# Kernel optimization log

Hardware: AMD Instinct MI355X
Metric: run time of the kernel (lower is better)

Reference implementation:

```python
import jax, jax.numpy as jnp
import numpy as np

B, T, C, NH = 2, 2048, 1024, 16
HD = C // NH  # 64


def _ln(x, g, b, eps=1e-5):
    m = x.mean(-1, keepdims=True)
    v = ((x - m) ** 2).mean(-1, keepdims=True)
    return (x - m) / jnp.sqrt(v + eps) * g + b


def _ff(x, w1, b1, w2, b2):
    # Linear -> exact (erf) GELU -> Linear; dropout=0 (identity)
    return jax.nn.gelu(x @ w1 + b1, approximate=False) @ w2 + b2


def setup_inputs() -> dict:
    key = jax.random.key(0)
    ks = jax.random.split(key, 16)
    s = 0.02
    f32 = jnp.float32
    return {
        "x": jax.random.normal(ks[0], (B, T, C), f32),
        # SelfAttn qkv projection (torch Linear stored transposed: (in, out))
        "w_attn": jax.random.normal(ks[1], (C, 3 * C), f32) * s,
        "b_attn": jnp.zeros((3 * C,), f32),
        # SelfAttn's internal FeedForward
        "wa1": jax.random.normal(ks[2], (C, 4 * C), f32) * s,
        "ba1": jnp.zeros((4 * C,), f32),
        "wa2": jax.random.normal(ks[3], (4 * C, C), f32) * s,
        "ba2": jnp.zeros((C,), f32),
        # Block ln1
        "g1": jnp.ones((C,), f32),
        "be1": jnp.zeros((C,), f32),
        # Block FeedForward
        "wf1": jax.random.normal(ks[4], (C, 4 * C), f32) * s,
        "bf1": jnp.zeros((4 * C,), f32),
        "wf2": jax.random.normal(ks[5], (4 * C, C), f32) * s,
        "bf2": jnp.zeros((C,), f32),
        # Block ln2
        "g2": jnp.ones((C,), f32),
        "be2": jnp.zeros((C,), f32),
    }


def reference(x, w_attn, b_attn, wa1, ba1, wa2, ba2, g1, be1,
              wf1, bf1, wf2, bf2, g2, be2):
    Bx, Tx, Cx = x.shape
    qkv = x @ w_attn + b_attn  # (B, T, 3C)
    # NOTE: original splits as K, Q, V (in that order)
    K, Q, V = jnp.split(qkv, 3, axis=-1)

    def heads(t):  # (B, T, C) -> (B, NH, T, HD)
        return t.reshape(Bx, Tx, NH, HD).transpose(0, 2, 1, 3)

    Q, K, V = heads(Q), heads(K), heads(V)
    att = jnp.einsum('bhqd,bhkd->bhqk', Q, K) / np.float32(np.sqrt(HD))
    mask = jnp.tril(jnp.ones((Tx, Tx), bool))  # causal
    att = jnp.where(mask, att, -jnp.inf)
    att = jax.nn.softmax(att, axis=-1)
    y = jnp.einsum('bhqk,bhkd->bhqd', att, V)
    y = y.transpose(0, 2, 1, 3).reshape(Bx, Tx, Cx)
    # SelfAttn applies its own FeedForward (no output projection)
    y = _ff(y, wa1, ba1, wa2, ba2)
    # Block: post-sublayer LayerNorm, additive residuals
    x = x + _ln(y, g1, be1)
    x = x + _ln(_ff(x, wf1, bf1, wf2, bf2), g2, be2)
    return x
```

## Files before the change

### kernel.cpp

```cpp
#include <hip/hip_runtime.h>
#include <hip/hip_bf16.h>
#include <math.h>

#define Bz 2
#define Tz 2048
#define Cz 1024
#define NHz 16
#define HDz 64
#define Mz (Bz*Tz)

typedef unsigned short u16;
typedef __attribute__((ext_vector_type(8))) short bf16x8;
typedef __attribute__((ext_vector_type(4))) float f32x4;

__device__ __forceinline__ float bf2f(u16 u){
  union { unsigned int i; float f; } v; v.i = ((unsigned int)u) << 16; return v.f;
}
__device__ __forceinline__ u16 f2bf(float f){
  union { float f; unsigned int i; } v; v.f = f;
  return (u16)((v.i + 0x7fffu + ((v.i >> 16) & 1u)) >> 16);
}
__device__ __forceinline__ unsigned pack_bf_trunc(float a, float b){
  union { float f; unsigned u; } ua, ub; ua.f = a; ub.f = b;
  return (ua.u >> 16) | (ub.u & 0xffff0000u);
}
__device__ __forceinline__ float gelu_fast(float x){
  float x3 = x * x * x;
  float z2 = 1.5957691216057308f * (x + 0.044715f * x3);
  float e  = __expf(z2);
  float t  = 1.f - 2.f / (e + 1.f);
  return 0.5f * x * (1.f + t);
}

__device__ __forceinline__ void glds16(const void* g, void* l){
  __builtin_amdgcn_global_load_lds(
      (const __attribute__((address_space(1))) void*)g,
      (__attribute__((address_space(3))) void*)l, 16, 0, 0);
}

__device__ __forceinline__ void pbar(){
  asm volatile("" ::: "memory");
  __builtin_amdgcn_s_barrier();
  asm volatile("" ::: "memory");
}
#define VMCNT(n) asm volatile("s_waitcnt vmcnt(" #n ")" ::: "memory")

__global__ __launch_bounds__(256) void cast4_kernel(const float* __restrict__ in,
                                                    u16* __restrict__ out, int n4){
  int i = blockIdx.x * 256 + threadIdx.x;
  if (i < n4) {
    float4 v = ((const float4*)in)[i];
    u16 t[4] = { f2bf(v.x), f2bf(v.y), f2bf(v.z), f2bf(v.w) };
    *(uint2*)&out[(size_t)i * 4] = *(const uint2*)t;
  }
}

__global__ __launch_bounds__(256) void transpose5_kernel(
    const float* __restrict__ s0, const float* __restrict__ s1,
    const float* __restrict__ s2, const float* __restrict__ s3,
    const float* __restrict__ s4,
    u16* __restrict__ d0, u16* __restrict__ d1, u16* __restrict__ d2,
    u16* __restrict__ d3, u16* __restrict__ d4){
  __shared__ float tile[32][33];
  const int t = blockIdx.x;
  const float* src; u16* dst; int K, N, local;
  if (t < 3072)       { src = s0; dst = d0; K = 1024; N = 3072; local = t; }
  else if (t < 7168)  { src = s1; dst = d1; K = 1024; N = 4096; local = t - 3072; }
  else if (t < 11264) { src = s2; dst = d2; K = 4096; N = 1024; local = t - 7168; }
  else if (t < 15360) { src = s3; dst = d3; K = 1024; N = 4096; local = t - 11264; }
  else                { src = s4; dst = d4; K = 4096; N = 1024; local = t - 15360; }
  const int NT = N >> 5;
  const int kb = (local / NT) * 32, nb = (local % NT) * 32;
  const int tx = threadIdx.x & 31, ty = threadIdx.x >> 5;
  #pragma unroll
  for (int r = ty; r < 32; r += 8)
    tile[r][tx] = src[(size_t)(kb + r) * N + nb + tx];
  __syncthreads();
  #pragma unroll
  for (int r = ty; r < 32; r += 8)
    dst[(size_t)(nb + r) * K + kb + tx] = f2bf(tile[tx][r]);
}

template<int ACT, int KLEN>
__global__ __launch_bounds__(512, 2) void gemm256_kernel(const u16* __restrict__ A,
                                                         const u16* __restrict__ Bt,
                                                         const float* __restrict__ bias,
                                                         u16* __restrict__ ob,
                                                         int N, int lda){
  __shared__ __align__(16) u16 As[2][256 * 64];
  __shared__ __align__(16) u16 Bs[2][256 * 64];
  const int tid  = threadIdx.x;
  const int lane = tid & 63;
  const int wave = tid >> 6;
  const int cc = lane & 15, quad = lane >> 4;
  const int wm = (wave >> 2) * 128;
  const int wn = (wave & 3) * 64;

  int flat = blockIdx.x + gridDim.x * blockIdx.y;
  const int nwg = gridDim.x * gridDim.y;
  flat = (flat & 7) * (nwg >> 3) + (flat >> 3);
  const int m0 = (flat & 15) * 256;
  const int n0 = (flat >> 4) * 256;

  const u16* Ak  = A  + (size_t)blockIdx.z * KLEN;
  const u16* Btk = Bt + (size_t)blockIdx.z * KLEN;

  int srow[2], scol[2];
  #pragma unroll
  for (int rnd = 0; rnd < 2; ++rnd) {
    const int ci = tid + rnd * 512;
    const int r = ci >> 3, cg = ci & 7;
    srow[rnd] = r;
    scol[rnd] = (cg ^ (r & 7)) * 8;
  }
  int colsw[2];
  #pragma unroll
  for (int s = 0; s < 2; ++s)
    colsw[s] = (s * 32 + quad * 8) ^ ((cc & 7) << 3);

  const auto stA = [&](int h, int t) {
    u16* dst = &As[t & 1][h * 8192];
    const u16* src = Ak + (size_t)(m0 + h * 128) * lda + t * 64;
    #pragma unroll
    for (int rnd = 0; rnd < 2; ++rnd)
      glds16(src + (size_t)srow[rnd] * lda + scol[rnd], dst + (tid + rnd * 512) * 8);
  };
  const auto stB = [&](int h, int t) {
    u16* dst = &Bs[t & 1][h * 8192];
    const u16* src = Btk + (size_t)(n0 + h * 128) * lda + t * 64;
    #pragma unroll
    for (int rnd = 0; rnd < 2; ++rnd)
      glds16(src + (size_t)srow[rnd] * lda + scol[rnd], dst + (tid + rnd * 512) * 8);
  };

  bf16x8 af[4][2];
  bf16x8 bfr[2][2][2];
  f32x4 acc[2][2][4][2] = {};

  const auto rdA = [&](int qa, int bsel) {
    #pragma unroll
    for (int f = 0; f < 4; ++f)
      #pragma unroll
      for (int s = 0; s < 2; ++s)
        af[f][s] = *(const bf16x8*)&As[bsel][(wm + qa * 64 + f * 16 + cc) * 64 + colsw[s]];
  };
  const auto rdB = [&](int qb, int bsel) {
    #pragma unroll
    for (int f = 0; f < 2; ++f)
      #pragma unroll
      for (int s = 0; s < 2; ++s)
        bfr[qb][f][s] = *(const bf16x8*)&Bs[bsel][(wn + qb * 32 + f * 16 + cc) * 64 + colsw[s]];
  };
  const auto mf16 = [&](int qa, int qb) {
    __builtin_amdgcn_s_setprio(1);
    #pragma unroll
    for (int s = 0; s < 2; ++s)
      #pragma unroll
      for (int am = 0; am < 4; ++am)
        #pragma unroll
        for (int bn = 0; bn < 2; ++bn)
          acc[qa][qb][am][bn] = __builtin_amdgcn_mfma_f32_16x16x32_bf16(
              af[am][s], bfr[qb][bn][s], acc[qa][qb][am][bn], 0, 0, 0);
    __builtin_amdgcn_s_setprio(0);
  };

  stB(0, 0); stB(1, 0); stA(0, 0); stA(1, 0);
  stB(0, 1); stB(1, 1);
  VMCNT(4);
  pbar();

  constexpr int nIter = KLEN >> 7;
  for (int i = 0; i < nIter; ++i) {
    const int t = 2 * i;
    const bool more = (i + 1 < nIter);
    rdA(0, 0); rdB(0, 0); stA(0, t + 1);
    pbar(); mf16(0, 0); pbar();
    rdB(1, 0); stA(1, t + 1);
    pbar(); mf16(0, 1); pbar();
    rdA(1, 0); if (more) stB(0, t + 2);
    pbar(); mf16(1, 1); pbar();
    if (more) stB(1, t + 2);
    pbar(); mf16(1, 0);
    if (more) { VMCNT(4); } else { VMCNT(0); }
    pbar();
    rdA(0, 1); rdB(0, 1); if (more) stA(0, t + 2);
    pbar(); mf16(0, 0); pbar();
    rdB(1, 1); if (more) stA(1, t + 2);
    pbar(); mf16(0, 1); pbar();
    rdA(1, 1); if (more) stB(0, t + 3);
    pbar(); mf16(1, 1); pbar();
    if (more) stB(1, t + 3);
    pbar(); mf16(1, 0);
    if (more) { VMCNT(4); }
    pbar();
  }

  u16* eb = (u16*)As;
  u16* obz = ob + (size_t)blockIdx.z * ((size_t)Mz * N);
  const float* bp = (blockIdx.z == 0) ? bias : nullptr;
  #pragma unroll
  for (int pass = 0; pass < 4; ++pass) {
    pbar();
    if (wm == (pass >> 1) * 128) {
      constexpr int dummy = 0; (void)dummy;
      const int qaa = pass & 1;
      #pragma unroll
      for (int qb = 0; qb < 2; ++qb)
        #pragma unroll
        for (int bn = 0; bn < 2; ++bn) {
          const int col = wn + qb * 32 + bn * 16 + cc;
          const float bv = bp ? bp[n0 + col] : 0.f;
          #pragma unroll
          for (int am = 0; am < 4; ++am)
            #pragma unroll
            for (int r = 0; r < 4; ++r) {
              const int rl = am * 16 + quad * 4 + r;
              float v = acc[qaa][qb][am][bn][r] + bv;
              if (ACT == 1) v = gelu_fast(v);
              eb[rl * 256 + (((col * 2) ^ ((rl & 7) << 4)) >> 1)] = f2bf(v);
            }
        }
    }
    pbar();
    #pragma unroll
    for (int c2 = 0; c2 < 4; ++c2) {
      const int byteoff = (tid + c2 * 512) * 16;
      const int rl = byteoff >> 9;
      const int cb = byteoff & 511;
      bf16x8 vv = *(const bf16x8*)((const char*)eb + rl * 512 + (cb ^ ((rl & 7) << 4)));
      *(bf16x8*)((char*)obz + ((size_t)(m0 + pass * 64 + rl) * N + n0) * 2 + cb) = vv;
    }
  }
}

__global__ __launch_bounds__(256) void vtrans_kernel(const u16* __restrict__ qkv,
                                                     u16* __restrict__ Vtb){
  __shared__ u16 Vl[64 * 72];
  const int tid = threadIdx.x;
  const int t0 = blockIdx.x * 64, h = blockIdx.y, b = blockIdx.z;
  const int bh = b * NHz + h;
  #pragma unroll
  for (int it = 0; it < 2; it++) {
    int c = tid + it * 256;
    int row = c >> 3, g = c & 7;
    *(uint4*)&Vl[row * 72 + g * 8] =
        *(const uint4*)(qkv + (size_t)(b * Tz + t0 + row) * (3 * Cz) + 2 * Cz + h * 64 + g * 8);
  }
  __syncthreads();
  #pragma unroll
  for (int it = 0; it < 2; it++) {
    int c = tid + it * 256;
    int d = c >> 3, tg = c & 7;
    u16 tmp[8];
    #pragma unroll
    for (int e = 0; e < 8; e++) tmp[e] = Vl[(tg * 8 + e) * 72 + d];
    *(uint4*)&Vtb[((size_t)bh * 64 + d) * Tz + t0 + tg * 8] = *(const uint4*)tmp;
  }
}

__global__ __launch_bounds__(256) void attn_kernel(const u16* __restrict__ qkv,
                                                   const u16* __restrict__ Vtb,
                                                   u16* __restrict__ y){
  __shared__ __align__(16) u16 KV[2][2][64 * 64];
  __shared__ __align__(16) u16 Ps[64 * 72];
  const int tid = threadIdx.x;
  const int lane = tid & 63, wave = tid >> 6;
  const int cc = lane & 15, quad = lane >> 4;
  const int flat = blockIdx.x;
  const int xcd = flat & 7, slot = flat >> 3;
  const int bhg = xcd * 4 + (slot >> 4);
  const int qtp = slot & 15;
  const int h = bhg & 15, b = bhg >> 4;
  const int bh = b * NHz + h;
  const size_t rowb = (size_t)b * Tz;
  const int wq0 = wave * 16;

  int foff[4][2];
  const int sw0 = (quad ^ (cc & 7)) * 8;
  const int sw1 = ((4 + quad) ^ (cc & 7)) * 8;
  #pragma unroll
  for (int t = 0; t < 4; ++t) {
    foff[t][0] = (t * 16 + cc) * 64 + sw0;
    foff[t][1] = (t * 16 + cc) * 64 + sw1;
  }
  const int pswb = (wq0 + cc) * 72 + quad * 4;
  const int psr0 = (wq0 + cc) * 72 + quad * 8;
  const int psr1 = (wq0 + cc) * 72 + 32 + quad * 8;

  auto stage = [&](int i, int bsel) {
    const int k0s = i * 64;
    #pragma unroll
    for (int it = 0; it < 2; ++it) {
      int ci = tid + it * 256;
      int row = ci >> 3, g = ci & 7;
      int gs = g ^ (row & 7);
      glds16(qkv + (rowb + k0s + row) * (3 * Cz) + h * 64 + gs * 8, &KV[bsel][0][ci * 8]);
      glds16(Vtb + ((size_t)bh * 64 + row) * Tz + k0s + gs * 8,     &KV[bsel][1][ci * 8]);
    }
  };

  for (int ph = 0; ph < 2; ++ph) {
    const int qt = ph ? (31 - qtp) : qtp;
    const int q0t = qt * 64 + wq0;
    const int nkt = qt + 1;
    const int wqmax = q0t + 15;

    bf16x8 qf[2];
    #pragma unroll
    for (int s = 0; s < 2; ++s)
      qf[s] = *(const bf16x8*)(qkv + (rowb + q0t + cc) * (3 * Cz)
                               + Cz + h * 64 + s * 32 + quad * 8);
    f32x4 acc[4] = {};
    float lp = 0.f;

    if (ph) __syncthreads();
    stage(0, 0);

    for (int i = 0; i < nkt; ++i) {
      __syncthreads();
      if (i + 1 < nkt) stage(i + 1, (i + 1) & 1);
      const int sel = i & 1;
      const u16* Kl = KV[sel][0];
      const u16* Vl = KV[sel][1];
      const int k0 = i * 64;
      if (k0 > wqmax) continue;

      bf16x8 kf[4][2];
      #pragma unroll
      for (int kt = 0; kt < 4; ++kt) {
        kf[kt][0] = *(const bf16x8*)&Kl[foff[kt][0]];
        kf[kt][1] = *(const bf16x8*)&Kl[foff[kt][1]];
      }
      const int qbase = q0t;
      #pragma unroll
      for (int kt = 0; kt < 4; ++kt) {
        const int kbase = k0 + kt * 16;
        uint2 pk;
        if (kbase > qbase + 15) {
          pk.x = 0u; pk.y = 0u;
        } else {
          f32x4 st = __builtin_amdgcn_mfma_f32_16x16x32_bf16(
              kf[kt][0], qf[0], (f32x4){0.f, 0.f, 0.f, 0.f}, 0, 0, 0);
          st = __builtin_amdgcn_mfma_f32_16x16x32_bf16(kf[kt][1], qf[1], st, 0, 0, 0);
          if (kbase + 15 > qbase) {
            const int kq = kbase + quad * 4, ql = qbase + cc;
            st[0] = (kq     <= ql) ? st[0] : -1e30f;
            st[1] = (kq + 1 <= ql) ? st[1] : -1e30f;
            st[2] = (kq + 2 <= ql) ? st[2] : -1e30f;
            st[3] = (kq + 3 <= ql) ? st[3] : -1e30f;
          }
          float p0 = __expf(fmaf(st[0], 0.125f, -16.f));
          float p1 = __expf(fmaf(st[1], 0.125f, -16.f));
          float p2 = __expf(fmaf(st[2], 0.125f, -16.f));
          float p3 = __expf(fmaf(st[3], 0.125f, -16.f));
          lp += (p0 + p1) + (p2 + p3);
          pk.x = pack_bf_trunc(p0, p1);
          pk.y = pack_bf_trunc(p2, p3);
        }
        *(uint2*)&Ps[pswb + kt * 16] = pk;
      }
      bf16x8 pf0 = *(const bf16x8*)&Ps[psr0];
      bf16x8 pf1 = *(const bf16x8*)&Ps[psr1];
      #pragma unroll
      for (int jd = 0; jd < 4; ++jd) {
        bf16x8 vf0 = *(const bf16x8*)&Vl[foff[jd][0]];
        bf16x8 vf1 = *(const bf16x8*)&Vl[foff[jd][1]];
        acc[jd] = __builtin_amdgcn_mfma_f32_16x16x32_bf16(pf0, vf0, acc[jd], 0, 0, 0);
        acc[jd] = __builtin_amdgcn_mfma_f32_16x16x32_bf16(pf1, vf1, acc[jd], 0, 0, 0);
      }
    }

    lp += __shfl_xor(lp, 16, 64);
    lp += __shfl_xor(lp, 32, 64);
    float inv[4];
    #pragma unroll
    for (int r = 0; r < 4; ++r) inv[r] = 1.f / __shfl(lp, quad * 4 + r, 64);
    #pragma unroll
    for (int jd = 0; jd < 4; ++jd)
      #pragma unroll
      for (int r = 0; r < 4; ++r) {
        int qrow = q0t + quad * 4 + r;
        y[(rowb + qrow) * Cz + h * 64 + jd * 16 + cc] = f2bf(acc[jd][r] * inv[r]);
      }
  }
}

__global__ __launch_bounds__(256) void ln_resid_kernel(const float* __restrict__ xf,
                                                       const u16* __restrict__ xb16,
                                                       const u16* __restrict__ yp,
                                                       const float* __restrict__ g,
                                                       const float* __restrict__ be,
                                                       float* __restrict__ outf,
                                                       u16* __restrict__ outb){
  const int row = blockIdx.x;
  const int c0 = threadIdx.x * 4;
  const size_t base = (size_t)row * Cz + c0;
  float4 v; v.x = 0.f; v.y = 0.f; v.z = 0.f; v.w = 0.f;
  #pragma unroll
  for (int p = 0; p < 4; ++p) {
    uint2 pp = *(const uint2*)(yp + (size_t)p * ((size_t)Mz * Cz) + base);
    v.x += bf2f((u16)(pp.x & 0xffff)); v.y += bf2f((u16)(pp.x >> 16));
    v.z += bf2f((u16)(pp.y & 0xffff)); v.w += bf2f((u16)(pp.y >> 16));
  }
  float s  = v.x + v.y + v.z + v.w;
  float s2 = v.x*v.x + v.y*v.y + v.z*v.z + v.w*v.w;
  #pragma unroll
  for (int off = 32; off > 0; off >>= 1) {
    s  += __shfl_down(s,  off);
    s2 += __shfl_down(s2, off);
  }
  __shared__ float ps[4], ps2[4];
  int wave = threadIdx.x >> 6, lane = threadIdx.x & 63;
  if (lane == 0) { ps[wave] = s; ps2[wave] = s2; }
  __syncthreads();
  s  = ps[0]  + ps[1]  + ps[2]  + ps[3];
  s2 = ps2[0] + ps2[1] + ps2[2] + ps2[3];
  const float mean = s * (1.f / Cz);
  const float var  = s2 * (1.f / Cz) - mean * mean;
  const float rstd = rsqrtf(var + 1e-5f);
  float4 xv;
  if (xf) {
    xv = *(const float4*)(xf + base);
  } else {
    uint2 px = *(const uint2*)(xb16 + base);
    xv.x = bf2f((u16)(px.x & 0xffff)); xv.y = bf2f((u16)(px.x >> 16));
    xv.z = bf2f((u16)(px.y & 0xffff)); xv.w = bf2f((u16)(px.y >> 16));
  }
  float4 gv = *(const float4*)(g + c0);
  float4 bv = *(const float4*)(be + c0);
  float4 ov;
  ov.x = xv.x + (v.x - mean) * rstd * gv.x + bv.x;
  ov.y = xv.y + (v.y - mean) * rstd * gv.y + bv.y;
  ov.z = xv.z + (v.z - mean) * rstd * gv.z + bv.z;
  ov.w = xv.w + (v.w - mean) * rstd * gv.w + bv.w;
  if (outf) *(float4*)(outf + base) = ov;
  if (outb) {
    u16 t[4] = { f2bf(ov.x), f2bf(ov.y), f2bf(ov.z), f2bf(ov.w) };
    *(ulonglong1*)&outb[base] = *(const ulonglong1*)t;
  }
}

extern "C" void kernel_launch(void* const* d_in, const int* in_sizes, int n_in,
                              void* d_out, int out_size, void* d_ws, size_t ws_size,
                              hipStream_t stream) {
  const float* x      = (const float*)d_in[0];
  const float* w_attn = (const float*)d_in[1];
  const float* b_attn = (const float*)d_in[2];
  const float* wa1    = (const float*)d_in[3];
  const float* ba1    = (const float*)d_in[4];
  const float* wa2    = (const float*)d_in[5];
  const float* ba2    = (const float*)d_in[6];
  const float* g1     = (const float*)d_in[7];
  const float* be1    = (const float*)d_in[8];
  const float* wf1    = (const float*)d_in[9];
  const float* bf1    = (const float*)d_in[10];
  const float* wf2    = (const float*)d_in[11];
  const float* bf2    = (const float*)d_in[12];
  const float* g2     = (const float*)d_in[13];
  const float* be2    = (const float*)d_in[14];
  float* out = (float*)d_out;

  char* ws = (char*)d_ws;
  size_t off = 0;
  auto alloc = [&](size_t bytes) { size_t o = off; off += (bytes + 255) & ~(size_t)255; return o; };
  u16* qkvb    = (u16*)(ws + alloc((size_t)Mz * 3 * Cz * 2));
  u16* ybuf    = (u16*)(ws + alloc((size_t)Mz * Cz * 2));
  u16* xb      = (u16*)(ws + alloc((size_t)Mz * Cz * 2));
  u16* wT_attn = (u16*)(ws + alloc((size_t)3 * Cz * Cz * 2));
  u16* wT_a1   = (u16*)(ws + alloc((size_t)4 * Cz * Cz * 2));
  u16* Vtb     = (u16*)(ws + alloc((size_t)Bz * NHz * HDz * Tz * 2));
  u16* wT_a2   = (u16*)(ws + alloc((size_t)4 * Cz * Cz * 2));
  u16* wT_f1   = (u16*)(ws + alloc((size_t)4 * Cz * Cz * 2));
  u16* wT_f2   = (u16*)(ws + alloc((size_t)4 * Cz * Cz * 2));
  u16* hbuf    = (u16*)(ws + alloc((size_t)Mz * 4 * Cz * 2));
  u16* pb      = (u16*)(ws + alloc((size_t)4 * Mz * Cz * 2));
  u16* x1b     = (u16*)(ws + alloc((size_t)Mz * Cz * 2));
  alloc(256);
  (void)ws_size; (void)in_sizes; (void)n_in; (void)out_size;

  cast4_kernel<<<(Mz * Cz / 4 + 255) / 256, 256, 0, stream>>>(x, xb, Mz * Cz / 4);
  transpose5_kernel<<<19456, 256, 0, stream>>>(w_attn, wa1, wa2, wf1, wf2,
                                               wT_attn, wT_a1, wT_a2, wT_f1, wT_f2);

  gemm256_kernel<0, Cz><<<dim3(16, 12, 1), 512, 0, stream>>>(xb, wT_attn, b_attn,
      qkvb, 3*Cz, Cz);

  vtrans_kernel<<<dim3(Tz/64, NHz, Bz), 256, 0, stream>>>(qkvb, Vtb);
  attn_kernel<<<dim3(512, 1, 1), 256, 0, stream>>>(qkvb, Vtb, ybuf);

  gemm256_kernel<1, Cz><<<dim3(16, 16, 1), 512, 0, stream>>>(ybuf, wT_a1, ba1,
      hbuf, 4*Cz, Cz);
  gemm256_kernel<0, Cz><<<dim3(16, 4, 4), 512, 0, stream>>>(hbuf, wT_a2, ba2,
      pb, Cz, 4*Cz);

  ln_resid_kernel<<<Mz, 256, 0, stream>>>(x, nullptr, pb, g1, be1,
                                          nullptr, x1b);

  gemm256_kernel<1, Cz><<<dim3(16, 16, 1), 512, 0, stream>>>(x1b, wT_f1, bf1,
      hbuf, 4*Cz, Cz);
  gemm256_kernel<0, Cz><<<dim3(16, 4, 4), 512, 0, stream>>>(hbuf, wT_f2, bf2,
      pb, Cz, 4*Cz);

  ln_resid_kernel<<<Mz, 256, 0, stream>>>(nullptr, x1b, pb, g2, be2,
                                          out, nullptr);
}
```

Baseline: 462.9 us.

## Merge prep kernels, coarsen GEMM pipeline phases, and store epilogue directly

The x cast kernel and the weight transpose kernel are merged into one launch. The GEMM main loop moves from four sub-phases per K-tile to two larger phases, issuing the loads for a whole tile at once and running 32 MFMAs between barriers, which halves the barrier count. The epilogue drops the LDS-staged coalesced store and writes bf16 values straight to global memory. That removes epilogue barriers but gives narrow 2-byte strided stores with poor coalescing, and the larger phases may raise register pressure.

New measurement: 443.7 us. -4.1%, faster.

```diff
diff --git a/kernel.cpp b/kernel.cpp
--- a/kernel.cpp
+++ b/kernel.cpp
@@ -45,24 +45,22 @@
 }
 #define VMCNT(n) asm volatile("s_waitcnt vmcnt(" #n ")" ::: "memory")
 
-__global__ __launch_bounds__(256) void cast4_kernel(const float* __restrict__ in,
-                                                    u16* __restrict__ out, int n4){
-  int i = blockIdx.x * 256 + threadIdx.x;
-  if (i < n4) {
-    float4 v = ((const float4*)in)[i];
-    u16 t[4] = { f2bf(v.x), f2bf(v.y), f2bf(v.z), f2bf(v.w) };
-    *(uint2*)&out[(size_t)i * 4] = *(const uint2*)t;
-  }
-}
-
-__global__ __launch_bounds__(256) void transpose5_kernel(
+__global__ __launch_bounds__(256) void prep_kernel(
+    const float* __restrict__ xin, u16* __restrict__ xout,
     const float* __restrict__ s0, const float* __restrict__ s1,
     const float* __restrict__ s2, const float* __restrict__ s3,
     const float* __restrict__ s4,
     u16* __restrict__ d0, u16* __restrict__ d1, u16* __restrict__ d2,
     u16* __restrict__ d3, u16* __restrict__ d4){
+  if (blockIdx.x < 4096) {
+    int i = blockIdx.x * 256 + threadIdx.x;
+    float4 v = ((const float4*)xin)[i];
+    u16 t[4] = { f2bf(v.x), f2bf(v.y), f2bf(v.z), f2bf(v.w) };
+    *(uint2*)&xout[(size_t)i * 4] = *(const uint2*)t;
+    return;
+  }
   __shared__ float tile[32][33];
-  const int t = blockIdx.x;
+  const int t = blockIdx.x - 4096;
   const float* src; u16* dst; int K, N, local;
   if (t < 3072)       { src = s0; dst = d0; K = 1024; N = 3072; local = t; }
   else if (t < 7168)  { src = s1; dst = d1; K = 1024; N = 4096; local = t - 3072; }
@@ -118,19 +116,25 @@
   for (int s = 0; s < 2; ++s)
     colsw[s] = (s * 32 + quad * 8) ^ ((cc & 7) << 3);
 
-  const auto stA = [&](int h, int t) {
-    u16* dst = &As[t & 1][h * 8192];
-    const u16* src = Ak + (size_t)(m0 + h * 128) * lda + t * 64;
-    #pragma unroll
-    for (int rnd = 0; rnd < 2; ++rnd)
-      glds16(src + (size_t)srow[rnd] * lda + scol[rnd], dst + (tid + rnd * 512) * 8);
-  };
-  const auto stB = [&](int h, int t) {
-    u16* dst = &Bs[t & 1][h * 8192];
-    const u16* src = Btk + (size_t)(n0 + h * 128) * lda + t * 64;
-    #pragma unroll
-    for (int rnd = 0; rnd < 2; ++rnd)
-      glds16(src + (size_t)srow[rnd] * lda + scol[rnd], dst + (tid + rnd * 512) * 8);
+  const auto stA = [&](int t) {
+    u16* dstb = As[t & 1];
+    const u16* src = Ak + (size_t)m0 * lda + t * 64;
+    #pragma unroll
+    for (int h = 0; h < 2; ++h)
+      #pragma unroll
+      for (int rnd = 0; rnd < 2; ++rnd)
+        glds16(src + (size_t)(h * 128 + srow[rnd]) * lda + scol[rnd],
+               dstb + h * 8192 + (tid + rnd * 512) * 8);
+  };
+  const auto stB = [&](int t) {
+    u16* dstb = Bs[t & 1];
+    const u16* src = Btk + (size_t)n0 * lda + t * 64;
+    #pragma unroll
+    for (int h = 0; h < 2; ++h)
+      #pragma unroll
+      for (int rnd = 0; rnd < 2; ++rnd)
+        glds16(src + (size_t)(h * 128 + srow[rnd]) * lda + scol[rnd],
+               dstb + h * 8192 + (tid + rnd * 512) * 8);
   };
 
   bf16x8 af[4][2];
@@ -151,21 +155,37 @@
       for (int s = 0; s < 2; ++s)
         bfr[qb][f][s] = *(const bf16x8*)&Bs[bsel][(wn + qb * 32 + f * 16 + cc) * 64 + colsw[s]];
   };
-  const auto mf16 = [&](int qa, int qb) {
+  const auto mf32 = [&](int qa) {
     __builtin_amdgcn_s_setprio(1);
     #pragma unroll
-    for (int s = 0; s < 2; ++s)
-      #pragma unroll
-      for (int am = 0; am < 4; ++am)
+    for (int qb = 0; qb < 2; ++qb)
+      #pragma unroll
+      for (int s = 0; s < 2; ++s)
         #pragma unroll
-        for (int bn = 0; bn < 2; ++bn)
-          acc[qa][qb][am][bn] = __builtin_amdgcn_mfma_f32_16x16x32_bf16(
-              af[am][s], bfr[qb][bn][s], acc[qa][qb][am][bn], 0, 0, 0);
+        for (int am = 0; am < 4; ++am)
+          #pragma unroll
+          for (int bn = 0; bn < 2; ++bn)
+            acc[qa][qb][am][bn] = __builtin_amdgcn_mfma_f32_16x16x32_bf16(
+                af[am][s], bfr[qb][bn][s], acc[qa][qb][am][bn], 0, 0, 0);
     __builtin_amdgcn_s_setprio(0);
   };
-
-  stB(0, 0); stB(1, 0); stA(0, 0); stA(1, 0);
-  stB(0, 1); stB(1, 1);
+  const auto mf32b = [&](int qa) {
+    __builtin_amdgcn_s_setprio(1);
+    #pragma unroll
+    for (int qb = 1; qb >= 0; --qb)
+      #pragma unroll
+      for (int s = 0; s < 2; ++s)
+        #pragma unroll
+        for (int am = 0; am < 4; ++am)
+          #pragma unroll
+          for (int bn = 0; bn < 2; ++bn)
+            acc[qa][qb][am][bn] = __builtin_amdgcn_mfma_f32_16x16x32_bf16(
+                af[am][s], bfr[qb][bn][s], acc[qa][qb][am][bn], 0, 0, 0);
+    __builtin_amdgcn_s_setprio(0);
+  };
+
+  stB(0); stA(0);
+  stB(1);
   VMCNT(4);
   pbar();
 
@@ -173,64 +193,41 @@
   for (int i = 0; i < nIter; ++i) {
     const int t = 2 * i;
     const bool more = (i + 1 < nIter);
-    rdA(0, 0); rdB(0, 0); stA(0, t + 1);
-    pbar(); mf16(0, 0); pbar();
-    rdB(1, 0); stA(1, t + 1);
-    pbar(); mf16(0, 1); pbar();
-    rdA(1, 0); if (more) stB(0, t + 2);
-    pbar(); mf16(1, 1); pbar();
-    if (more) stB(1, t + 2);
-    pbar(); mf16(1, 0);
+    rdA(0, 0); rdB(0, 0); rdB(1, 0); stA(t + 1);
+    pbar(); mf32(0); pbar();
+    rdA(1, 0); if (more) stB(t + 2);
+    pbar(); mf32b(1);
     if (more) { VMCNT(4); } else { VMCNT(0); }
     pbar();
-    rdA(0, 1); rdB(0, 1); if (more) stA(0, t + 2);
-    pbar(); mf16(0, 0); pbar();
-    rdB(1, 1); if (more) stA(1, t + 2);
-    pbar(); mf16(0, 1); pbar();
-    rdA(1, 1); if (more) stB(0, t + 3);
-    pbar(); mf16(1, 1); pbar();
-    if (more) stB(1, t + 3);
-    pbar(); mf16(1, 0);
+    rdA(0, 1); rdB(0, 1); rdB(1, 1); if (more) stA(t + 2);
+    pbar(); mf32(0); pbar();
+    rdA(1, 1); if (more) stB(t + 3);
+    pbar(); mf32b(1);
     if (more) { VMCNT(4); }
     pbar();
   }
 
-  u16* eb = (u16*)As;
   u16* obz = ob + (size_t)blockIdx.z * ((size_t)Mz * N);
   const float* bp = (blockIdx.z == 0) ? bias : nullptr;
-  #pragma unroll
-  for (int pass = 0; pass < 4; ++pass) {
-    pbar();
-    if (wm == (pass >> 1) * 128) {
-      constexpr int dummy = 0; (void)dummy;
-      const int qaa = pass & 1;
-      #pragma unroll
-      for (int qb = 0; qb < 2; ++qb)
+  const int rbase = quad * 4;
+  #pragma unroll
+  for (int qa = 0; qa < 2; ++qa)
+    #pragma unroll
+    for (int qb = 0; qb < 2; ++qb)
+      #pragma unroll
+      for (int bn = 0; bn < 2; ++bn) {
+        const int col = n0 + wn + qb * 32 + bn * 16 + cc;
+        const float bv = bp ? bp[col] : 0.f;
         #pragma unroll
-        for (int bn = 0; bn < 2; ++bn) {
-          const int col = wn + qb * 32 + bn * 16 + cc;
-          const float bv = bp ? bp[n0 + col] : 0.f;
+        for (int am = 0; am < 4; ++am)
           #pragma unroll
-          for (int am = 0; am < 4; ++am)
-            #pragma unroll
-            for (int r = 0; r < 4; ++r) {
-              const int rl = am * 16 + quad * 4 + r;
-              float v = acc[qaa][qb][am][bn][r] + bv;
-              if (ACT == 1) v = gelu_fast(v);
-              eb[rl * 256 + (((col * 2) ^ ((rl & 7) << 4)) >> 1)] = f2bf(v);
-            }
-        }
-    }
-    pbar();
-    #pragma unroll
-    for (int c2 = 0; c2 < 4; ++c2) {
-      const int byteoff = (tid + c2 * 512) * 16;
-      const int rl = byteoff >> 9;
-      const int cb = byteoff & 511;
-      bf16x8 vv = *(const bf16x8*)((const char*)eb + rl * 512 + (cb ^ ((rl & 7) << 4)));
-      *(bf16x8*)((char*)obz + ((size_t)(m0 + pass * 64 + rl) * N + n0) * 2 + cb) = vv;
-    }
-  }
+          for (int r = 0; r < 4; ++r) {
+            const int row = m0 + wm + qa * 64 + am * 16 + rbase + r;
+            float v = acc[qa][qb][am][bn][r] + bv;
+            if (ACT == 1) v = gelu_fast(v);
+            obz[(size_t)row * N + col] = f2bf(v);
+          }
+      }
 }
 
 __global__ __launch_bounds__(256) void vtrans_kernel(const u16* __restrict__ qkv,
@@ -478,9 +475,8 @@
   alloc(256);
   (void)ws_size; (void)in_sizes; (void)n_in; (void)out_size;
 
-  cast4_kernel<<<(Mz * Cz / 4 + 255) / 256, 256, 0, stream>>>(x, xb, Mz * Cz / 4);
-  transpose5_kernel<<<19456, 256, 0, stream>>>(w_attn, wa1, wa2, wf1, wf2,
-                                               wT_attn, wT_a1, wT_a2, wT_f1, wT_f2);
+  prep_kernel<<<4096 + 19456, 256, 0, stream>>>(x, xb, w_attn, wa1, wa2, wf1, wf2,
+                                                wT_attn, wT_a1, wT_a2, wT_f1, wT_f2);
 
   gemm256_kernel<0, Cz><<<dim3(16, 12, 1), 512, 0, stream>>>(xb, wT_attn, b_attn,
       qkvb, 3*Cz, Cz);
```
